# Performance work log

Measured on AMD Instinct MI355X. Metric: run time of the kernel, lower is better.

Reference implementation:

```python
import jax, jax.numpy as jnp
import numpy as np

GROUPS = 32
HEADS = 8
EPS = 1e-5

def setup_inputs() -> dict:
    key = jax.random.key(0)
    ks = jax.random.split(key, 5)
    C = 512
    x = jax.random.normal(ks[0], (8, C, 32, 32), dtype=jnp.float32)
    gn_w = jnp.ones((C,), dtype=jnp.float32)
    gn_b = jnp.zeros((C,), dtype=jnp.float32)
    qkv_w = jax.random.normal(ks[1], (3 * C, C), dtype=jnp.float32) * 0.02
    qkv_b = jnp.zeros((3 * C,), dtype=jnp.float32)
    proj_w = jax.random.normal(ks[2], (C, C), dtype=jnp.float32) * 0.02
    proj_b = jnp.zeros((C,), dtype=jnp.float32)
    return {"x": x, "gn_w": gn_w, "gn_b": gn_b, "qkv_w": qkv_w,
            "qkv_b": qkv_b, "proj_w": proj_w, "proj_b": proj_b}

def reference(x, gn_w, gn_b, qkv_w, qkv_b, proj_w, proj_b):
    B, C, H, W = x.shape
    d = C // HEADS
    # GroupNorm(32, C)
    xg = x.reshape(B, GROUPS, C // GROUPS, H, W)
    mean = xg.mean(axis=(2, 3, 4), keepdims=True)
    var = xg.var(axis=(2, 3, 4), keepdims=True)
    h = ((xg - mean) * jax.lax.rsqrt(var + EPS)).reshape(B, C, H, W)
    h = h * gn_w[None, :, None, None] + gn_b[None, :, None, None]
    # 1x1 conv QKV == channel matmul
    qkv = jnp.einsum('bchw,oc->bohw', h, qkv_w) + qkv_b[None, :, None, None]
    qkv = qkv.reshape(B, 3, HEADS, d, H * W)
    q, k, v = qkv[:, 0], qkv[:, 1], qkv[:, 2]  # [B, heads, d, HW]
    scale = d ** (-0.5)
    # weight[b,h,q,k] = sum_d q[b,h,d,q] * k[b,h,d,k] * scale
    attn = jax.nn.softmax(jnp.einsum('bhdq,bhdk->bhqk', q, k) * scale, axis=-1)
    # out[b,h,d,q] = sum_k v[b,h,d,k] * attn[b,h,q,k]
    out = jnp.einsum('bhdk,bhqk->bhdq', v, attn).reshape(B, C, H, W)
    out = jnp.einsum('bchw,oc->bohw', out, proj_w) + proj_b[None, :, None, None]
    return out + x
```

## Files before the change

kernel.cpp:

```cpp
#include <hip/hip_runtime.h>
#include <math.h>

#define B_    8
#define C_    512
#define HW_   1024
#define O3_   1536
#define HEADS_ 8
#define D_    64
#define G_    32
#define CPG_  16
#define EPS_  1e-5f
#define M_TOT 8192

#define QSCALE (0.125f * 1.44269504088896f)

typedef __bf16 bf16x8 __attribute__((ext_vector_type(8)));
typedef __bf16 bf16x4 __attribute__((ext_vector_type(4)));
typedef float  f32x4  __attribute__((ext_vector_type(4)));

__device__ __forceinline__ void async_copy16(void* lds, const void* g) {
  __builtin_amdgcn_global_load_lds(
      (const __attribute__((address_space(1))) unsigned int*)g,
      (__attribute__((address_space(3))) unsigned int*)lds, 16, 0, 0);
}

__global__ __launch_bounds__(256) void k_gn(const float* __restrict__ x,
                                            const float* __restrict__ gw,
                                            const float* __restrict__ gb,
                                            __bf16* __restrict__ h,
                                            const float* __restrict__ qw,
                                            const float* __restrict__ pw,
                                            __bf16* __restrict__ qwb,
                                            __bf16* __restrict__ pwb) {
  __shared__ float red[10];
  __shared__ __bf16 T[16 * 1030];
  if (blockIdx.x >= B_ * G_) {
    int i = (blockIdx.x - B_ * G_) * 256 + threadIdx.x;
    if (i < O3_ * C_) qwb[i] = (__bf16)qw[i];
    if (i < C_ * C_)  pwb[i] = (__bf16)pw[i];
    return;
  }
  int bg = blockIdx.x;
  int b = bg >> 5, g = bg & 31;
  const float* xg = x + ((size_t)(b * C_) + g * CPG_) * HW_;
  int tid = threadIdx.x;

  float s = 0.f, ss = 0.f;
  for (int i = tid; i < CPG_ * HW_; i += 256) {
    float v = xg[i];
    s += v; ss += v * v;
  }
  for (int off = 32; off > 0; off >>= 1) {
    s  += __shfl_down(s, off, 64);
    ss += __shfl_down(ss, off, 64);
  }
  int wv = tid >> 6;
  if ((tid & 63) == 0) { red[wv] = s; red[4 + wv] = ss; }
  __syncthreads();
  if (tid == 0) {
    float S  = red[0] + red[1] + red[2] + red[3];
    float SS = red[4] + red[5] + red[6] + red[7];
    float mean = S / (float)(CPG_ * HW_);
    float var  = SS / (float)(CPG_ * HW_) - mean * mean;
    red[8] = mean;
    red[9] = rsqrtf(var + EPS_);
  }
  __syncthreads();
  float mean = red[8], rstd = red[9];

  for (int i = tid; i < CPG_ * HW_; i += 256) {
    int c = i >> 10, hw = i & 1023;
    float ga = gw[g * CPG_ + c], be = gb[g * CPG_ + c];
    float v = xg[i];
    T[c * 1030 + hw] = (__bf16)((v - mean) * rstd * ga + be);
  }
  __syncthreads();

  __bf16* hb = h + (size_t)b * HW_ * C_ + g * CPG_;
  for (int j = tid; j < CPG_ * HW_; j += 256) {
    int hw = j >> 4, c = j & 15;
    hb[(size_t)hw * C_ + c] = T[c * 1030 + hw];
  }
}

#define BK 64
__device__ __forceinline__ void gemm128_core(const __bf16* __restrict__ aBase,
                                             const __bf16* __restrict__ bBase,
                                             __bf16* As, __bf16* Bs,
                                             f32x4 acc[4][4]) {
  int t = threadIdx.x;
  int lane = t & 63;
  int l16 = lane & 15, quad = lane >> 4;
  int wv = t >> 6;
  int wm = (wv >> 1) * 64, wn = (wv & 1) * 64;

  int rsub = lane >> 3;
  int chunk = (lane & 7) ^ rsub;
  const __bf16* ag = aBase + (size_t)(wv * 32 + rsub) * C_ + chunk * 8;
  const __bf16* bg = bBase + (size_t)(wv * 32 + rsub) * C_ + chunk * 8;
  __bf16* la = As + wv * 2048 + lane * 8;
  __bf16* lb = Bs + wv * 2048 + lane * 8;
  int sw = l16 & 7;

  for (int k0 = 0; k0 < C_; k0 += BK) {
#pragma unroll
    for (int s = 0; s < 4; s++) {
      async_copy16(la + s * 512, ag + (size_t)(s * 8) * C_ + k0);
      async_copy16(lb + s * 512, bg + (size_t)(s * 8) * C_ + k0);
    }
    __syncthreads();
#pragma unroll
    for (int h = 0; h < 2; h++) {
      bf16x8 af[4], bf[4];
#pragma unroll
      for (int i = 0; i < 4; i++) {
        af[i] = *(const bf16x8*)(As + (wm + i * 16 + l16) * BK +
                                 ((h * 4 + quad) ^ sw) * 8);
        bf[i] = *(const bf16x8*)(Bs + (wn + i * 16 + l16) * BK +
                                 ((h * 4 + quad) ^ sw) * 8);
      }
#pragma unroll
      for (int i = 0; i < 4; i++)
#pragma unroll
        for (int j = 0; j < 4; j++)
          acc[i][j] = __builtin_amdgcn_mfma_f32_16x16x32_bf16(af[i], bf[j],
                                                              acc[i][j], 0, 0, 0);
    }
    __syncthreads();
  }
}

__global__ __launch_bounds__(256) void k_qkv(const __bf16* __restrict__ h,
                                             const __bf16* __restrict__ w,
                                             const float* __restrict__ bias,
                                             __bf16* __restrict__ y) {
  __shared__ __align__(16) __bf16 As[128 * BK];
  __shared__ __align__(16) __bf16 Bs[128 * BK];
  int m0 = blockIdx.x * 128, n0 = blockIdx.y * 128;
  f32x4 acc[4][4];
#pragma unroll
  for (int i = 0; i < 4; i++)
#pragma unroll
    for (int j = 0; j < 4; j++) acc[i][j] = f32x4{0.f, 0.f, 0.f, 0.f};
  gemm128_core(h + (size_t)m0 * C_, w + (size_t)n0 * C_, As, Bs, acc);

  float sc = (n0 < C_) ? QSCALE : 1.0f;
  int lane = threadIdx.x & 63, wv = threadIdx.x >> 6;
  int l16 = lane & 15, quad = lane >> 4;
  int wm = (wv >> 1) * 64, wn = (wv & 1) * 64;
#pragma unroll
  for (int j = 0; j < 4; j++) {
    int n = n0 + wn + j * 16 + l16;
    float bv = bias[n];
#pragma unroll
    for (int i = 0; i < 4; i++)
#pragma unroll
      for (int r = 0; r < 4; r++) {
        int m = m0 + wm + i * 16 + quad * 4 + r;
        y[(size_t)m * O3_ + n] = (__bf16)((acc[i][j][r] + bv) * sc);
      }
  }
}

__global__ __launch_bounds__(256) void k_vt(const __bf16* __restrict__ y,
                                            __bf16* __restrict__ vT) {
  __shared__ __bf16 T[64 * 66];
  int b = blockIdx.z, ct = blockIdx.y, tt = blockIdx.x;
  int t = threadIdx.x;
  int tok0 = tt * 64, c0 = ct * 64;
  const __bf16* src = y + ((size_t)(b * HW_ + tok0)) * O3_ + 2 * C_ + c0;
#pragma unroll
  for (int r = 0; r < 2; r++) {
    int tok = r * 32 + (t >> 3);
    int cc = (t & 7) * 8;
    bf16x8 v = *(const bf16x8*)(src + (size_t)tok * O3_ + cc);
#pragma unroll
    for (int j = 0; j < 8; j++) T[(cc + j) * 66 + tok] = v[j];
  }
  __syncthreads();
  __bf16* dst = vT + ((size_t)(b * C_) + c0) * HW_ + tok0;
#pragma unroll
  for (int r = 0; r < 2; r++) {
    int cc = r * 32 + (t >> 3);
    int tk = (t & 7) * 8;
    *(bf16x8*)(dst + (size_t)cc * HW_ + tk) = *(const bf16x8*)(&T[cc * 66 + tk]);
  }
}

__global__ __launch_bounds__(256) void k_attn(const __bf16* __restrict__ y,
                                              const __bf16* __restrict__ vT,
                                              __bf16* __restrict__ ao) {
  __shared__ __align__(16) __bf16 Ks[128 * 64];
  __shared__ __align__(16) __bf16 Vt[64 * 128];
  __shared__ __align__(16) __bf16 Pp[4][32 * 136];
  int hd = blockIdx.x, b = blockIdx.y, qt = blockIdx.z;
  int t = threadIdx.x;
  int wv = t >> 6, lane = t & 63, l16 = lane & 15, quad = lane >> 4;
  int q0 = qt * 128 + wv * 32;

  const __bf16* base = y + (size_t)(b * HW_) * O3_ + hd * D_;
  const __bf16* kg = base + C_;
  const __bf16* vtg = vT + ((size_t)(b * C_) + hd * D_) * HW_;

  bf16x8 qb[2][2];
#pragma unroll
  for (int qg = 0; qg < 2; qg++)
#pragma unroll
    for (int dh = 0; dh < 2; dh++)
      qb[qg][dh] = *(const bf16x8*)(base + (size_t)(q0 + qg * 16 + l16) * O3_ +
                                    dh * 32 + quad * 8);

  int kRowSub = lane >> 3;
  int kChunk = (lane & 7) ^ (kRowSub & 7);

  float l_run[2] = {0.f, 0.f};
  f32x4 o_acc[4][2];
#pragma unroll
  for (int dt = 0; dt < 4; dt++)
#pragma unroll
    for (int qg = 0; qg < 2; qg++) o_acc[dt][qg] = f32x4{0.f, 0.f, 0.f, 0.f};

  for (int kt = 0; kt < HW_; kt += 128) {
#pragma unroll
    for (int s = 0; s < 4; s++) {
      int row = wv * 32 + s * 8 + kRowSub;
      async_copy16(Ks + (wv * 32 + s * 8) * 64 + lane * 8,
                   kg + (size_t)(kt + row) * O3_ + kChunk * 8);
    }
#pragma unroll
    for (int s = 0; s < 4; s++) {
      int row = wv * 16 + s * 4 + (lane >> 4);
      int c2 = (lane & 15) ^ (row & 15);
      async_copy16(Vt + (wv * 16 + s * 4) * 128 + lane * 8,
                   vtg + (size_t)row * HW_ + kt + c2 * 8);
    }
    __syncthreads();

    f32x4 st[8][2];
#pragma unroll
    for (int tt = 0; tt < 8; tt++) {
      int row = tt * 16 + l16;
      bf16x8 ka0 = *(const bf16x8*)(&Ks[row * 64 + ((quad) ^ (l16 & 7)) * 8]);
      bf16x8 ka1 = *(const bf16x8*)(&Ks[row * 64 + ((4 + quad) ^ (l16 & 7)) * 8]);
      f32x4 z = {0.f, 0.f, 0.f, 0.f};
      st[tt][0] = __builtin_amdgcn_mfma_f32_16x16x32_bf16(ka0, qb[0][0], z, 0, 0, 0);
      st[tt][0] = __builtin_amdgcn_mfma_f32_16x16x32_bf16(ka1, qb[0][1], st[tt][0], 0, 0, 0);
      st[tt][1] = __builtin_amdgcn_mfma_f32_16x16x32_bf16(ka0, qb[1][0], z, 0, 0, 0);
      st[tt][1] = __builtin_amdgcn_mfma_f32_16x16x32_bf16(ka1, qb[1][1], st[tt][1], 0, 0, 0);
    }

#pragma unroll
    for (int qg = 0; qg < 2; qg++) {
      float rs = 0.f;
#pragma unroll
      for (int tt = 0; tt < 8; tt++)
#pragma unroll
        for (int r = 0; r < 4; r++) {
          float e = exp2f(st[tt][qg][r]);
          st[tt][qg][r] = e;
          rs += e;
        }
      rs += __shfl_xor(rs, 16, 64);
      rs += __shfl_xor(rs, 32, 64);
      l_run[qg] += rs;
    }

#pragma unroll
    for (int qg = 0; qg < 2; qg++)
#pragma unroll
      for (int tt = 0; tt < 8; tt++) {
        bf16x4 pk;
#pragma unroll
        for (int r = 0; r < 4; r++) pk[r] = (__bf16)st[tt][qg][r];
        *(bf16x4*)(&Pp[wv][(qg * 16 + l16) * 136 + tt * 16 + quad * 4]) = pk;
      }
    asm volatile("s_waitcnt lgkmcnt(0)" ::: "memory");

#pragma unroll
    for (int kh = 0; kh < 4; kh++) {
      bf16x8 pb0 = *(const bf16x8*)(&Pp[wv][l16 * 136 + kh * 32 + quad * 8]);
      bf16x8 pb1 = *(const bf16x8*)(&Pp[wv][(16 + l16) * 136 + kh * 32 + quad * 8]);
#pragma unroll
      for (int dt = 0; dt < 4; dt++) {
        int vpos = ((kh * 4 + quad) ^ l16) * 8;
        bf16x8 va = *(const bf16x8*)(&Vt[(dt * 16 + l16) * 128 + vpos]);
        o_acc[dt][0] = __builtin_amdgcn_mfma_f32_16x16x32_bf16(va, pb0, o_acc[dt][0], 0, 0, 0);
        o_acc[dt][1] = __builtin_amdgcn_mfma_f32_16x16x32_bf16(va, pb1, o_acc[dt][1], 0, 0, 0);
      }
    }
    __syncthreads();
  }

  float inv0 = 1.f / l_run[0], inv1 = 1.f / l_run[1];
#pragma unroll
  for (int dt = 0; dt < 4; dt++)
#pragma unroll
    for (int r = 0; r < 4; r++) {
      int ch = hd * D_ + dt * 16 + quad * 4 + r;
      ao[(size_t)(b * HW_ + q0 + l16) * C_ + ch] = (__bf16)(o_acc[dt][0][r] * inv0);
      ao[(size_t)(b * HW_ + q0 + 16 + l16) * C_ + ch] = (__bf16)(o_acc[dt][1][r] * inv1);
    }
}

__global__ __launch_bounds__(256) void k_proj(const __bf16* __restrict__ ao,
                                              const __bf16* __restrict__ w,
                                              const float* __restrict__ bias,
                                              const float* __restrict__ x,
                                              float* __restrict__ out) {
  __shared__ __align__(16) __bf16 As[128 * BK];
  __shared__ __align__(16) __bf16 Bs[128 * BK];
  int n0 = blockIdx.x * 128, m0 = blockIdx.y * 128;
  f32x4 acc[4][4];
#pragma unroll
  for (int i = 0; i < 4; i++)
#pragma unroll
    for (int j = 0; j < 4; j++) acc[i][j] = f32x4{0.f, 0.f, 0.f, 0.f};
  gemm128_core(w + (size_t)m0 * C_, ao + (size_t)n0 * C_, As, Bs, acc);

  int lane = threadIdx.x & 63, wv = threadIdx.x >> 6;
  int l16 = lane & 15, quad = lane >> 4;
  int wm = (wv >> 1) * 64, wn = (wv & 1) * 64;
#pragma unroll
  for (int i = 0; i < 4; i++)
#pragma unroll
    for (int r = 0; r < 4; r++) {
      int o = m0 + wm + i * 16 + quad * 4 + r;
      float bv = bias[o];
#pragma unroll
      for (int j = 0; j < 4; j++) {
        int n = n0 + wn + j * 16 + l16;
        int b = n >> 10, hw = n & 1023;
        size_t idx = ((size_t)(b * C_ + o)) * HW_ + hw;
        out[idx] = acc[i][j][r] + bv + x[idx];
      }
    }
}

extern "C" void kernel_launch(void* const* d_in, const int* in_sizes, int n_in,
                              void* d_out, int out_size, void* d_ws, size_t ws_size,
                              hipStream_t stream) {
  const float* x      = (const float*)d_in[0];
  const float* gn_w   = (const float*)d_in[1];
  const float* gn_b   = (const float*)d_in[2];
  const float* qkv_w  = (const float*)d_in[3];
  const float* qkv_b  = (const float*)d_in[4];
  const float* proj_w = (const float*)d_in[5];
  const float* proj_b = (const float*)d_in[6];
  float* out = (float*)d_out;

  char* ws = (char*)d_ws;
  __bf16* h   = (__bf16*)(ws);
  __bf16* vT  = (__bf16*)(ws);
  __bf16* qwb = (__bf16*)(ws + 8388608);
  __bf16* pwb = (__bf16*)(ws + 8388608 + 1572864);
  __bf16* yq  = (__bf16*)(ws + 8388608 + 1572864 + 524288);
  __bf16* ao  = (__bf16*)(ws + 8388608 + 1572864 + 524288 + 25165824);

  int cvtBlocks = (O3_ * C_ + 255) / 256;
  k_gn  <<<B_ * G_ + cvtBlocks, 256, 0, stream>>>(x, gn_w, gn_b, h,
                                                  qkv_w, proj_w, qwb, pwb);
  k_qkv <<<dim3(M_TOT / 128, O3_ / 128, 1), 256, 0, stream>>>(h, qwb, qkv_b, yq);
  k_vt  <<<dim3(16, 8, B_), 256, 0, stream>>>(yq, vT);
  k_attn<<<dim3(HEADS_, B_, 8), 256, 0, stream>>>(yq, vT, ao);
  k_proj<<<dim3(M_TOT / 128, C_ / 128, 1), 256, 0, stream>>>(ao, pwb, proj_b, x, out);
  (void)in_sizes; (void)n_in; (void)out_size; (void)ws_size;
}
```

Baseline: 175.6 us.

## Fuse V transpose into QKV GEMM epilogue and vectorize attention output stores

The QKV GEMM epilogue now writes the V block straight into the transposed vT layout with 4-wide bf16 stores, so the separate k_vt transpose kernel, its launch and its extra read and write of V are gone. vT gets its own workspace region because it can no longer alias h, which the GEMM is still reading. In the attention kernel the cross-lane shuffle reduction of the softmax row sum moves out of the key loop and runs once at the end, and the output writes become bf16x4 vector stores. The strided vT stores from the GEMM epilogue may coalesce less well than the old LDS-tiled transpose did.

```diff
diff --git a/kernel.cpp b/kernel.cpp
--- a/kernel.cpp
+++ b/kernel.cpp
@@ -133,7 +133,8 @@
 __global__ __launch_bounds__(256) void k_qkv(const __bf16* __restrict__ h,
                                              const __bf16* __restrict__ w,
                                              const float* __restrict__ bias,
-                                             __bf16* __restrict__ y) {
+                                             __bf16* __restrict__ y,
+                                             __bf16* __restrict__ vT) {
   __shared__ __align__(16) __bf16 As[128 * BK];
   __shared__ __align__(16) __bf16 Bs[128 * BK];
   int m0 = blockIdx.x * 128, n0 = blockIdx.y * 128;
@@ -144,46 +145,41 @@
     for (int j = 0; j < 4; j++) acc[i][j] = f32x4{0.f, 0.f, 0.f, 0.f};
   gemm128_core(h + (size_t)m0 * C_, w + (size_t)n0 * C_, As, Bs, acc);
 
-  float sc = (n0 < C_) ? QSCALE : 1.0f;
   int lane = threadIdx.x & 63, wv = threadIdx.x >> 6;
   int l16 = lane & 15, quad = lane >> 4;
   int wm = (wv >> 1) * 64, wn = (wv & 1) * 64;
-#pragma unroll
-  for (int j = 0; j < 4; j++) {
-    int n = n0 + wn + j * 16 + l16;
-    float bv = bias[n];
-#pragma unroll
-    for (int i = 0; i < 4; i++)
-#pragma unroll
-      for (int r = 0; r < 4; r++) {
-        int m = m0 + wm + i * 16 + quad * 4 + r;
-        y[(size_t)m * O3_ + n] = (__bf16)((acc[i][j][r] + bv) * sc);
-      }
-  }
-}
-
-__global__ __launch_bounds__(256) void k_vt(const __bf16* __restrict__ y,
-                                            __bf16* __restrict__ vT) {
-  __shared__ __bf16 T[64 * 66];
-  int b = blockIdx.z, ct = blockIdx.y, tt = blockIdx.x;
-  int t = threadIdx.x;
-  int tok0 = tt * 64, c0 = ct * 64;
-  const __bf16* src = y + ((size_t)(b * HW_ + tok0)) * O3_ + 2 * C_ + c0;
-#pragma unroll
-  for (int r = 0; r < 2; r++) {
-    int tok = r * 32 + (t >> 3);
-    int cc = (t & 7) * 8;
-    bf16x8 v = *(const bf16x8*)(src + (size_t)tok * O3_ + cc);
-#pragma unroll
-    for (int j = 0; j < 8; j++) T[(cc + j) * 66 + tok] = v[j];
-  }
-  __syncthreads();
-  __bf16* dst = vT + ((size_t)(b * C_) + c0) * HW_ + tok0;
-#pragma unroll
-  for (int r = 0; r < 2; r++) {
-    int cc = r * 32 + (t >> 3);
-    int tk = (t & 7) * 8;
-    *(bf16x8*)(dst + (size_t)cc * HW_ + tk) = *(const bf16x8*)(&T[cc * 66 + tk]);
+
+  if (n0 >= 2 * C_) {
+    int bb = m0 >> 10;
+    int tokBase = (m0 & 1023) + wm + quad * 4;
+#pragma unroll
+    for (int j = 0; j < 4; j++) {
+      int n = n0 + wn + j * 16 + l16;
+      int c = n - 2 * C_;
+      float bv = bias[n];
+      __bf16* vrow = vT + ((size_t)(bb * C_) + c) * HW_;
+#pragma unroll
+      for (int i = 0; i < 4; i++) {
+        bf16x4 pk;
+#pragma unroll
+        for (int r = 0; r < 4; r++) pk[r] = (__bf16)(acc[i][j][r] + bv);
+        *(bf16x4*)(vrow + tokBase + i * 16) = pk;
+      }
+    }
+  } else {
+    float sc = (n0 < C_) ? QSCALE : 1.0f;
+#pragma unroll
+    for (int j = 0; j < 4; j++) {
+      int n = n0 + wn + j * 16 + l16;
+      float bv = bias[n];
+#pragma unroll
+      for (int i = 0; i < 4; i++)
+#pragma unroll
+        for (int r = 0; r < 4; r++) {
+          int m = m0 + wm + i * 16 + quad * 4 + r;
+          y[(size_t)m * O3_ + n] = (__bf16)((acc[i][j][r] + bv) * sc);
+        }
+    }
   }
 }
 
@@ -260,8 +256,6 @@
           st[tt][qg][r] = e;
           rs += e;
         }
-      rs += __shfl_xor(rs, 16, 64);
-      rs += __shfl_xor(rs, 32, 64);
       l_run[qg] += rs;
     }
 
@@ -291,15 +285,25 @@
     __syncthreads();
   }
 
+#pragma unroll
+  for (int qg = 0; qg < 2; qg++) {
+    l_run[qg] += __shfl_xor(l_run[qg], 16, 64);
+    l_run[qg] += __shfl_xor(l_run[qg], 32, 64);
+  }
   float inv0 = 1.f / l_run[0], inv1 = 1.f / l_run[1];
-#pragma unroll
-  for (int dt = 0; dt < 4; dt++)
+
+#pragma unroll
+  for (int dt = 0; dt < 4; dt++) {
+    bf16x4 p0, p1;
 #pragma unroll
     for (int r = 0; r < 4; r++) {
-      int ch = hd * D_ + dt * 16 + quad * 4 + r;
-      ao[(size_t)(b * HW_ + q0 + l16) * C_ + ch] = (__bf16)(o_acc[dt][0][r] * inv0);
-      ao[(size_t)(b * HW_ + q0 + 16 + l16) * C_ + ch] = (__bf16)(o_acc[dt][1][r] * inv1);
-    }
+      p0[r] = (__bf16)(o_acc[dt][0][r] * inv0);
+      p1[r] = (__bf16)(o_acc[dt][1][r] * inv1);
+    }
+    int ch = hd * D_ + dt * 16 + quad * 4;
+    *(bf16x4*)(ao + (size_t)(b * HW_ + q0 + l16) * C_ + ch) = p0;
+    *(bf16x4*)(ao + (size_t)(b * HW_ + q0 + 16 + l16) * C_ + ch) = p1;
+  }
 }
 
 __global__ __launch_bounds__(256) void k_proj(const __bf16* __restrict__ ao,
@@ -350,17 +354,16 @@
 
   char* ws = (char*)d_ws;
   __bf16* h   = (__bf16*)(ws);
-  __bf16* vT  = (__bf16*)(ws);
   __bf16* qwb = (__bf16*)(ws + 8388608);
   __bf16* pwb = (__bf16*)(ws + 8388608 + 1572864);
   __bf16* yq  = (__bf16*)(ws + 8388608 + 1572864 + 524288);
   __bf16* ao  = (__bf16*)(ws + 8388608 + 1572864 + 524288 + 25165824);
+  __bf16* vT  = (__bf16*)(ws + 8388608 + 1572864 + 524288 + 25165824 + 8388608);
 
   int cvtBlocks = (O3_ * C_ + 255) / 256;
   k_gn  <<<B_ * G_ + cvtBlocks, 256, 0, stream>>>(x, gn_w, gn_b, h,
                                                   qkv_w, proj_w, qwb, pwb);
-  k_qkv <<<dim3(M_TOT / 128, O3_ / 128, 1), 256, 0, stream>>>(h, qwb, qkv_b, yq);
-  k_vt  <<<dim3(16, 8, B_), 256, 0, stream>>>(yq, vT);
+  k_qkv <<<dim3(M_TOT / 128, O3_ / 128, 1), 256, 0, stream>>>(h, qwb, qkv_b, yq, vT);
   k_attn<<<dim3(HEADS_, B_, 8), 256, 0, stream>>>(yq, vT, ao);
   k_proj<<<dim3(M_TOT / 128, C_ / 128, 1), 256, 0, stream>>>(ao, pwb, proj_b, x, out);
   (void)in_sizes; (void)n_in; (void)out_size; (void)ws_size;
```

Result: faster. 170.2 us (-3.1%).
